# Kernel optimization log

Measured on AMD Instinct MI355X. Metric: run time of the kernel, lower is better.

Reference implementation:

```python
import jax, jax.numpy as jnp
import numpy as np

B, SQ, SK, D = 8, 4096, 4096, 64


def setup_inputs() -> dict:
    key = jax.random.key(0)
    k1, k2, k3 = jax.random.split(key, 3)
    x1 = jax.random.normal(k1, (B, SQ, D), dtype=jnp.float32)   # queries
    x2 = jax.random.normal(k2, (B, SK, D), dtype=jnp.float32)   # keys
    x3 = jax.random.normal(k3, (B, SK, D), dtype=jnp.float32)   # values
    x4 = 0                                                      # dropout p (static, 0 => deterministic)
    x5 = jnp.ones((1,), dtype=jnp.float32)                      # scale divisor
    return {"x1": x1, "x2": x2, "x3": x3, "x4": x4, "x5": x5}


def reference(x1, x2, x3, x4, x5):
    # scores: [B, Sq, Sk]
    scores = jnp.einsum("bqd,bkd->bqk", x1, x2) / x5
    attn = jax.nn.softmax(scores, axis=-1)
    p = float(x4)  # static python scalar
    if p > 0.0:
        mask = jax.random.bernoulli(jax.random.key(42), 1.0 - p, attn.shape)
        attn = attn * mask.astype(attn.dtype) / (1.0 - p)
    # out: [B, Sq, D]
    return jnp.einsum("bqk,bkd->bqd", attn, x3)
```

## Files before the change

kernel.cpp:

```cpp
#include <hip/hip_runtime.h>


typedef _Float16 f16x8 __attribute__((ext_vector_type(8)));
typedef _Float16 f16x4 __attribute__((ext_vector_type(4)));
typedef __fp16   h16x2 __attribute__((ext_vector_type(2)));
typedef float    f32x4 __attribute__((ext_vector_type(4)));
typedef float    f32x16 __attribute__((ext_vector_type(16)));

constexpr int kB  = 8;
constexpr int kSQ = 4096;
constexpr int kSK = 4096;
constexpr int kD  = 64;
constexpr int KSPLIT = 4;
constexpr int SKH = kSK / KSPLIT;
constexpr int BQ  = 128;
constexpr int BK  = 64;
constexpr size_t APART = (size_t)kB * kSQ * kD;
constexpr float kLog2e = 1.44269504088896340736f;

static __device__ __forceinline__ f16x4 pack4(float a, float b, float c, float d) {
    h16x2 p0 = __builtin_amdgcn_cvt_pkrtz(a, b);
    h16x2 p1 = __builtin_amdgcn_cvt_pkrtz(c, d);
    f16x4 r;
    r[0] = (_Float16)p0[0]; r[1] = (_Float16)p0[1];
    r[2] = (_Float16)p1[0]; r[3] = (_Float16)p1[1];
    return r;
}
static __device__ __forceinline__ f16x8 pack8(const float4& a, const float4& c) {
    f16x4 lo = pack4(a.x, a.y, a.z, a.w);
    f16x4 hi = pack4(c.x, c.y, c.z, c.w);
    f16x8 f;
    f[0] = lo[0]; f[1] = lo[1]; f[2] = lo[2]; f[3] = lo[3];
    f[4] = hi[0]; f[5] = hi[1]; f[6] = hi[2]; f[7] = hi[3];
    return f;
}
static __device__ __forceinline__ unsigned pkrtz_u(float a, float b) {
    union { h16x2 h; unsigned u; } cv;
    cv.h = __builtin_amdgcn_cvt_pkrtz(a, b);
    return cv.u;
}

typedef const __attribute__((address_space(1))) unsigned int* gu32p;
typedef __attribute__((address_space(3))) unsigned int* lu32p;
static __device__ __forceinline__ void gload_lds16(const void* g, void* l) {
    __builtin_amdgcn_global_load_lds((gu32p)g, (lu32p)l, 16, 0, 0);
}

#define PA_SLICE(dst, sv, rb) do {                                          \
    unsigned c0 = pkrtz_u((sv)[(rb)+0], (sv)[(rb)+1]);                      \
    unsigned c1 = pkrtz_u((sv)[(rb)+2], (sv)[(rb)+3]);                      \
    unsigned c2 = pkrtz_u((sv)[(rb)+4], (sv)[(rb)+5]);                      \
    unsigned c3 = pkrtz_u((sv)[(rb)+6], (sv)[(rb)+7]);                      \
    auto r02 = __builtin_amdgcn_permlane32_swap(c0, c2, false, false);      \
    auto r13 = __builtin_amdgcn_permlane32_swap(c1, c3, false, false);      \
    union { unsigned u[4]; f16x8 v; } _r;                                   \
    _r.u[0] = r02[0]; _r.u[1] = r13[0]; _r.u[2] = r02[1]; _r.u[3] = r13[1]; \
    dst = _r.v;                                                             \
} while (0)

__global__ __launch_bounds__(256, 2)
void fattn_prepass(const float* __restrict__ Kg,
                   const float* __restrict__ Vg,
                   _Float16* __restrict__ Kh,
                   _Float16* __restrict__ Vt)
{
    __shared__ _Float16 tr[kD][BK];

    const int tid = threadIdx.x;
    const int kt  = blockIdx.x;
    const int b   = blockIdx.y;

    const int k = tid >> 2;
    const int p = tid & 3;
    const int gk = kt * BK + k;

    {
        const float* src = Kg + ((size_t)b * kSK + gk) * kD + p * 16;
        const float4 a0 = *(const float4*)(src + 0);
        const float4 a1 = *(const float4*)(src + 4);
        const float4 a2 = *(const float4*)(src + 8);
        const float4 a3 = *(const float4*)(src + 12);
        _Float16* dst = Kh + ((size_t)b * kSK + gk) * kD;
        const int fb0 = 2 * p, fb1 = 2 * p + 1;
        *(f16x8*)&dst[(fb0 ^ (gk & 7)) * 8] = pack8(a0, a1);
        *(f16x8*)&dst[(fb1 ^ (gk & 7)) * 8] = pack8(a2, a3);
    }
    {
        const float* src = Vg + ((size_t)b * kSK + gk) * kD + p * 16;
        const float4 a0 = *(const float4*)(src + 0);
        const float4 a1 = *(const float4*)(src + 4);
        const float4 a2 = *(const float4*)(src + 8);
        const float4 a3 = *(const float4*)(src + 12);
        const float v[16] = {a0.x,a0.y,a0.z,a0.w, a1.x,a1.y,a1.z,a1.w,
                             a2.x,a2.y,a2.z,a2.w, a3.x,a3.y,a3.z,a3.w};
#pragma unroll
        for (int j = 0; j < 16; ++j)
            tr[p * 16 + j][k] = (_Float16)v[j];
    }
    __syncthreads();
    {
        const int f  = tid >> 2;
        const int p2 = tid & 3;
        const f16x8 b0 = *(const f16x8*)&tr[f][p2 * 16 + 0];
        const f16x8 b1 = *(const f16x8*)&tr[f][p2 * 16 + 8];
        _Float16* dst = Vt + (((size_t)b * 64 + kt) * kD + f) * BK;
        const int kb0 = 2 * p2, kb1 = 2 * p2 + 1;
        *(f16x8*)&dst[(kb0 ^ (f & 7)) * 8] = b0;
        *(f16x8*)&dst[(kb1 ^ (f & 7)) * 8] = b1;
    }
}

__global__ __launch_bounds__(256, 4)
void fattn_partial(const float* __restrict__ Qg,
                   const _Float16* __restrict__ Kh,
                   const _Float16* __restrict__ Vt,
                   const float* __restrict__ sdiv,
                   _Float16* __restrict__ Ap,
                   float2* __restrict__ MLp)
{
    __shared__ __align__(16) _Float16 sK[2][BK * kD];
    __shared__ __align__(16) _Float16 sV[2][kD * BK];

    const int tid  = threadIdx.x;
    const int w    = tid >> 6;
    const int lane = tid & 63;
    const int l31  = lane & 31;
    const int hi   = lane >> 5;

    const int flat = blockIdx.x;
    const int c    = flat & 31;
    const int qi   = flat >> 5;
    const int b    = c >> 2;
    const int ks   = c & 3;
    const int qb   = qi * BQ;

    const float qscale = kLog2e / sdiv[0];

    const float* Qb = Qg + ((size_t)b * kSQ + qb) * kD;
    const _Float16* Khb = Kh + ((size_t)b * kSK + (size_t)ks * SKH) * kD;
    const _Float16* Vtb = Vt + (((size_t)b * 64 + (size_t)ks * (SKH / BK)) * kD) * BK;

    f16x8 qf[4];
    {
        const float* qrow = Qb + (size_t)(w * 32 + l31) * kD;
#pragma unroll
        for (int ds = 0; ds < 4; ++ds) {
            const float4 a  = *(const float4*)(qrow + ds * 16 + hi * 8);
            const float4 cc = *(const float4*)(qrow + ds * 16 + hi * 8 + 4);
            float4 as = make_float4(a.x * qscale, a.y * qscale, a.z * qscale, a.w * qscale);
            float4 cs = make_float4(cc.x * qscale, cc.y * qscale, cc.z * qscale, cc.w * qscale);
            qf[ds] = pack8(as, cs);
        }
    }

    int offA[4];
#pragma unroll
    for (int i = 0; i < 4; ++i)
        offA[i] = l31 * 64 + (((2 * i + hi) ^ (l31 & 7)) * 8);

    auto stage = [&](int kt, int buf) {
        const char* gk = (const char*)(Khb + (size_t)kt * BK * kD) + w * 2048 + lane * 16;
        const char* gv = (const char*)(Vtb + (size_t)kt * kD * BK) + w * 2048 + lane * 16;
        char* lk = (char*)&sK[buf][0] + w * 2048;
        char* lv = (char*)&sV[buf][0] + w * 2048;
        gload_lds16(gk,        lk);
        gload_lds16(gk + 1024, lk + 1024);
        gload_lds16(gv,        lv);
        gload_lds16(gv + 1024, lv + 1024);
    };

    f32x16 o0, o1;
#pragma unroll
    for (int r = 0; r < 16; ++r) { o0[r] = 0.0f; o1[r] = 0.0f; }
    float m_i = -1e30f;
    float ll  = 0.0f;

    stage(0, 0);
    __syncthreads();

    const int nIter = SKH / BK;
    for (int kt = 0; kt < nIter; ++kt) {
        const int buf = kt & 1;
        if (kt + 1 < nIter) stage(kt + 1, buf ^ 1);

        f32x16 s0, s1;
#pragma unroll
        for (int r = 0; r < 16; ++r) { s0[r] = 0.0f; s1[r] = 0.0f; }
#pragma unroll
        for (int ds = 0; ds < 4; ++ds) {
            const f16x8 kf0 = *(const f16x8*)&sK[buf][offA[ds]];
            const f16x8 kf1 = *(const f16x8*)&sK[buf][offA[ds] + 2048];
            s0 = __builtin_amdgcn_mfma_f32_32x32x16_f16(kf0, qf[ds], s0, 0, 0, 0);
            s1 = __builtin_amdgcn_mfma_f32_32x32x16_f16(kf1, qf[ds], s1, 0, 0, 0);
        }

        f16x8 vf[4][2];
#pragma unroll
        for (int s = 0; s < 4; ++s) {
            vf[s][0] = *(const f16x8*)&sV[buf][offA[s]];
            vf[s][1] = *(const f16x8*)&sV[buf][offA[s] + 2048];
        }

        float t[16];
#pragma unroll
        for (int r = 0; r < 16; ++r) t[r] = fmaxf(s0[r], s1[r]);
#pragma unroll
        for (int r = 0; r < 8; ++r)  t[r] = fmaxf(t[r], t[r + 8]);
#pragma unroll
        for (int r = 0; r < 4; ++r)  t[r] = fmaxf(t[r], t[r + 4]);
        float rm = fmaxf(fmaxf(t[0], t[1]), fmaxf(t[2], t[3]));
        rm = fmaxf(rm, __shfl_xor(rm, 32, 64));
        const float mnew = fmaxf(m_i, rm);

#pragma unroll
        for (int r = 0; r < 16; ++r) {
            s0[r] = __builtin_amdgcn_exp2f(s0[r] - mnew);
            s1[r] = __builtin_amdgcn_exp2f(s1[r] - mnew);
        }
        if (!__all(mnew == m_i)) {
            const float alpha = __builtin_amdgcn_exp2f(m_i - mnew);
            ll *= alpha;
#pragma unroll
            for (int r = 0; r < 16; ++r) { o0[r] *= alpha; o1[r] *= alpha; }
        }
        m_i = mnew;

        {
            float a0 = 0.f, a1 = 0.f, a2 = 0.f, a3 = 0.f;
#pragma unroll
            for (int r = 0; r < 16; r += 4) {
                a0 += s0[r]; a1 += s0[r + 1]; a2 += s0[r + 2]; a3 += s0[r + 3];
                a0 += s1[r]; a1 += s1[r + 1]; a2 += s1[r + 2]; a3 += s1[r + 3];
            }
            ll += (a0 + a1) + (a2 + a3);
        }

        f16x8 pa[4];
        PA_SLICE(pa[0], s0, 0);
        PA_SLICE(pa[1], s0, 8);
        PA_SLICE(pa[2], s1, 0);
        PA_SLICE(pa[3], s1, 8);

#pragma unroll
        for (int s = 0; s < 4; ++s) {
            o0 = __builtin_amdgcn_mfma_f32_32x32x16_f16(vf[s][0], pa[s], o0, 0, 0, 0);
            o1 = __builtin_amdgcn_mfma_f32_32x32x16_f16(vf[s][1], pa[s], o1, 0, 0, 0);
        }

        __syncthreads();
    }

    _Float16* Ab = Ap + (size_t)ks * APART + ((size_t)b * kSQ + qb) * kD;
    float2* MLb = MLp + (size_t)ks * kB * kSQ + (size_t)b * kSQ + qb;
    const int q = w * 32 + l31;
    _Float16* arow = &Ab[(size_t)q * kD];
#pragma unroll
    for (int g = 0; g < 4; ++g) {
        *(f16x4*)&arow[g * 8 + hi * 4] =
            pack4(o0[4 * g], o0[4 * g + 1], o0[4 * g + 2], o0[4 * g + 3]);
        *(f16x4*)&arow[32 + g * 8 + hi * 4] =
            pack4(o1[4 * g], o1[4 * g + 1], o1[4 * g + 2], o1[4 * g + 3]);
    }
    {
        const float lf = ll + __shfl_xor(ll, 32, 64);
        if (hi == 0) MLb[q] = make_float2(m_i, lf);
    }
}

__global__ __launch_bounds__(256)
void fattn_combine(const _Float16* __restrict__ Ap,
                   const float2* __restrict__ MLp,
                   float* __restrict__ Og)
{
    const int idx = blockIdx.x * 256 + threadIdx.x;
    const int r = idx >> 4;
    const int c = (idx & 15) * 4;

    float m = -1e30f;
    float2 ml[KSPLIT];
#pragma unroll
    for (int s = 0; s < KSPLIT; ++s) {
        ml[s] = MLp[(size_t)s * kB * kSQ + r];
        m = fmaxf(m, ml[s].x);
    }
    float acc[4] = {0.f, 0.f, 0.f, 0.f};
    float lsum = 0.f;
#pragma unroll
    for (int s = 0; s < KSPLIT; ++s) {
        const float e = __builtin_amdgcn_exp2f(ml[s].x - m);
        lsum += e * ml[s].y;
        const f16x4 a = *(const f16x4*)&Ap[(size_t)s * APART + (size_t)r * kD + c];
#pragma unroll
        for (int j = 0; j < 4; ++j) acc[j] += e * (float)a[j];
    }
    const float inv = 1.0f / lsum;
    float4 res = make_float4(acc[0] * inv, acc[1] * inv, acc[2] * inv, acc[3] * inv);
    *(float4*)&Og[(size_t)r * kD + c] = res;
}

extern "C" void kernel_launch(void* const* d_in, const int* in_sizes, int n_in,
                              void* d_out, int out_size, void* d_ws, size_t ws_size,
                              hipStream_t stream) {
    const float* Q    = (const float*)d_in[0];
    const float* K    = (const float*)d_in[1];
    const float* V    = (const float*)d_in[2];
    const float* sdiv = (const float*)d_in[4];
    float* O = (float*)d_out;

    _Float16* Kh  = (_Float16*)d_ws;
    _Float16* Vt  = Kh + (size_t)kB * kSK * kD;
    _Float16* Ap  = Vt + (size_t)kB * kSK * kD;
    float2*   MLp = (float2*)(Ap + (size_t)KSPLIT * APART);

    fattn_prepass<<<dim3(kSK / BK, kB), dim3(256), 0, stream>>>(K, V, Kh, Vt);
    fattn_partial<<<dim3((kSQ / BQ) * kB * KSPLIT), dim3(256), 0, stream>>>(Q, Kh, Vt, sdiv, Ap, MLp);
    fattn_combine<<<dim3(kB * kSQ * kD / (256 * 4)), dim3(256), 0, stream>>>(Ap, MLp, O);
}
```

Before: 143.0 us.

## Double query tile per wave and defer softmax rescaling with a threshold

Each wave now processes two 32-row query tiles (BQ 256), reusing the V fragments loaded from LDS across both tiles and halving the number of workgroups. Online-softmax rescaling is skipped unless the new row max exceeds the running max by a threshold, which cuts rescale work and branch cost. Partial outputs are normalized before the fp16 store, and combine weights by exp*l so the fp16 partials stay in range. The cost is higher register pressure (occupancy hint lowered from 4 to 2), fewer blocks in flight, and K fragments are still reloaded per tile.

After: 135.0 us. 1.06x faster.

```diff
diff --git a/kernel.cpp b/kernel.cpp
--- a/kernel.cpp
+++ b/kernel.cpp
@@ -13,10 +13,12 @@
 constexpr int kD  = 64;
 constexpr int KSPLIT = 4;
 constexpr int SKH = kSK / KSPLIT;
-constexpr int BQ  = 128;
+constexpr int BQ  = 256;
+constexpr int MT  = 2;
 constexpr int BK  = 64;
 constexpr size_t APART = (size_t)kB * kSQ * kD;
 constexpr float kLog2e = 1.44269504088896340736f;
+constexpr float kDeferThr = 11.5f;
 
 static __device__ __forceinline__ f16x4 pack4(float a, float b, float c, float d) {
     h16x2 p0 = __builtin_amdgcn_cvt_pkrtz(a, b);
@@ -110,7 +112,7 @@
     }
 }
 
-__global__ __launch_bounds__(256, 4)
+__global__ __launch_bounds__(256, 2)
 void fattn_partial(const float* __restrict__ Qg,
                    const _Float16* __restrict__ Kh,
                    const _Float16* __restrict__ Vt,
@@ -140,16 +142,17 @@
     const _Float16* Khb = Kh + ((size_t)b * kSK + (size_t)ks * SKH) * kD;
     const _Float16* Vtb = Vt + (((size_t)b * 64 + (size_t)ks * (SKH / BK)) * kD) * BK;
 
-    f16x8 qf[4];
-    {
-        const float* qrow = Qb + (size_t)(w * 32 + l31) * kD;
+    f16x8 qf[MT][4];
+#pragma unroll
+    for (int mt = 0; mt < MT; ++mt) {
+        const float* qrow = Qb + (size_t)(w * 64 + mt * 32 + l31) * kD;
 #pragma unroll
         for (int ds = 0; ds < 4; ++ds) {
             const float4 a  = *(const float4*)(qrow + ds * 16 + hi * 8);
             const float4 cc = *(const float4*)(qrow + ds * 16 + hi * 8 + 4);
             float4 as = make_float4(a.x * qscale, a.y * qscale, a.z * qscale, a.w * qscale);
             float4 cs = make_float4(cc.x * qscale, cc.y * qscale, cc.z * qscale, cc.w * qscale);
-            qf[ds] = pack8(as, cs);
+            qf[mt][ds] = pack8(as, cs);
         }
     }
 
@@ -169,11 +172,14 @@
         gload_lds16(gv + 1024, lv + 1024);
     };
 
-    f32x16 o0, o1;
-#pragma unroll
-    for (int r = 0; r < 16; ++r) { o0[r] = 0.0f; o1[r] = 0.0f; }
-    float m_i = -1e30f;
-    float ll  = 0.0f;
+    f32x16 oL[MT], oH[MT];
+    float m_i[MT], ll[MT];
+#pragma unroll
+    for (int mt = 0; mt < MT; ++mt) {
+        m_i[mt] = -1e30f; ll[mt] = 0.0f;
+#pragma unroll
+        for (int r = 0; r < 16; ++r) { oL[mt][r] = 0.0f; oH[mt][r] = 0.0f; }
+    }
 
     stage(0, 0);
     __syncthreads();
@@ -183,17 +189,6 @@
         const int buf = kt & 1;
         if (kt + 1 < nIter) stage(kt + 1, buf ^ 1);
 
-        f32x16 s0, s1;
-#pragma unroll
-        for (int r = 0; r < 16; ++r) { s0[r] = 0.0f; s1[r] = 0.0f; }
-#pragma unroll
-        for (int ds = 0; ds < 4; ++ds) {
-            const f16x8 kf0 = *(const f16x8*)&sK[buf][offA[ds]];
-            const f16x8 kf1 = *(const f16x8*)&sK[buf][offA[ds] + 2048];
-            s0 = __builtin_amdgcn_mfma_f32_32x32x16_f16(kf0, qf[ds], s0, 0, 0, 0);
-            s1 = __builtin_amdgcn_mfma_f32_32x32x16_f16(kf1, qf[ds], s1, 0, 0, 0);
-        }
-
         f16x8 vf[4][2];
 #pragma unroll
         for (int s = 0; s < 4; ++s) {
@@ -201,50 +196,65 @@
             vf[s][1] = *(const f16x8*)&sV[buf][offA[s] + 2048];
         }
 
-        float t[16];
-#pragma unroll
-        for (int r = 0; r < 16; ++r) t[r] = fmaxf(s0[r], s1[r]);
-#pragma unroll
-        for (int r = 0; r < 8; ++r)  t[r] = fmaxf(t[r], t[r + 8]);
-#pragma unroll
-        for (int r = 0; r < 4; ++r)  t[r] = fmaxf(t[r], t[r + 4]);
-        float rm = fmaxf(fmaxf(t[0], t[1]), fmaxf(t[2], t[3]));
-        rm = fmaxf(rm, __shfl_xor(rm, 32, 64));
-        const float mnew = fmaxf(m_i, rm);
-
-#pragma unroll
-        for (int r = 0; r < 16; ++r) {
-            s0[r] = __builtin_amdgcn_exp2f(s0[r] - mnew);
-            s1[r] = __builtin_amdgcn_exp2f(s1[r] - mnew);
-        }
-        if (!__all(mnew == m_i)) {
-            const float alpha = __builtin_amdgcn_exp2f(m_i - mnew);
-            ll *= alpha;
-#pragma unroll
-            for (int r = 0; r < 16; ++r) { o0[r] *= alpha; o1[r] *= alpha; }
-        }
-        m_i = mnew;
-
-        {
-            float a0 = 0.f, a1 = 0.f, a2 = 0.f, a3 = 0.f;
-#pragma unroll
-            for (int r = 0; r < 16; r += 4) {
-                a0 += s0[r]; a1 += s0[r + 1]; a2 += s0[r + 2]; a3 += s0[r + 3];
-                a0 += s1[r]; a1 += s1[r + 1]; a2 += s1[r + 2]; a3 += s1[r + 3];
-            }
-            ll += (a0 + a1) + (a2 + a3);
-        }
-
-        f16x8 pa[4];
-        PA_SLICE(pa[0], s0, 0);
-        PA_SLICE(pa[1], s0, 8);
-        PA_SLICE(pa[2], s1, 0);
-        PA_SLICE(pa[3], s1, 8);
-
-#pragma unroll
-        for (int s = 0; s < 4; ++s) {
-            o0 = __builtin_amdgcn_mfma_f32_32x32x16_f16(vf[s][0], pa[s], o0, 0, 0, 0);
-            o1 = __builtin_amdgcn_mfma_f32_32x32x16_f16(vf[s][1], pa[s], o1, 0, 0, 0);
+#pragma unroll
+        for (int mt = 0; mt < MT; ++mt) {
+            f32x16 s0, s1;
+#pragma unroll
+            for (int r = 0; r < 16; ++r) { s0[r] = 0.0f; s1[r] = 0.0f; }
+#pragma unroll
+            for (int ds = 0; ds < 4; ++ds) {
+                const f16x8 kf0 = *(const f16x8*)&sK[buf][offA[ds]];
+                const f16x8 kf1 = *(const f16x8*)&sK[buf][offA[ds] + 2048];
+                s0 = __builtin_amdgcn_mfma_f32_32x32x16_f16(kf0, qf[mt][ds], s0, 0, 0, 0);
+                s1 = __builtin_amdgcn_mfma_f32_32x32x16_f16(kf1, qf[mt][ds], s1, 0, 0, 0);
+            }
+
+            float t[16];
+#pragma unroll
+            for (int r = 0; r < 16; ++r) t[r] = fmaxf(s0[r], s1[r]);
+#pragma unroll
+            for (int r = 0; r < 8; ++r)  t[r] = fmaxf(t[r], t[r + 8]);
+#pragma unroll
+            for (int r = 0; r < 4; ++r)  t[r] = fmaxf(t[r], t[r + 4]);
+            float rm = fmaxf(fmaxf(t[0], t[1]), fmaxf(t[2], t[3]));
+            rm = fmaxf(rm, __shfl_xor(rm, 32, 64));
+
+            if (!__all(rm <= m_i[mt] + kDeferThr)) {
+                const float mnew  = fmaxf(m_i[mt], rm);
+                const float alpha = __builtin_amdgcn_exp2f(m_i[mt] - mnew);
+                ll[mt] *= alpha;
+#pragma unroll
+                for (int r = 0; r < 16; ++r) { oL[mt][r] *= alpha; oH[mt][r] *= alpha; }
+                m_i[mt] = mnew;
+            }
+
+#pragma unroll
+            for (int r = 0; r < 16; ++r) {
+                s0[r] = __builtin_amdgcn_exp2f(s0[r] - m_i[mt]);
+                s1[r] = __builtin_amdgcn_exp2f(s1[r] - m_i[mt]);
+            }
+
+            {
+                float a0 = 0.f, a1 = 0.f, a2 = 0.f, a3 = 0.f;
+#pragma unroll
+                for (int r = 0; r < 16; r += 4) {
+                    a0 += s0[r]; a1 += s0[r + 1]; a2 += s0[r + 2]; a3 += s0[r + 3];
+                    a0 += s1[r]; a1 += s1[r + 1]; a2 += s1[r + 2]; a3 += s1[r + 3];
+                }
+                ll[mt] += (a0 + a1) + (a2 + a3);
+            }
+
+            f16x8 pa[4];
+            PA_SLICE(pa[0], s0, 0);
+            PA_SLICE(pa[1], s0, 8);
+            PA_SLICE(pa[2], s1, 0);
+            PA_SLICE(pa[3], s1, 8);
+
+#pragma unroll
+            for (int s = 0; s < 4; ++s) {
+                oL[mt] = __builtin_amdgcn_mfma_f32_32x32x16_f16(vf[s][0], pa[s], oL[mt], 0, 0, 0);
+                oH[mt] = __builtin_amdgcn_mfma_f32_32x32x16_f16(vf[s][1], pa[s], oH[mt], 0, 0, 0);
+            }
         }
 
         __syncthreads();
@@ -252,18 +262,22 @@
 
     _Float16* Ab = Ap + (size_t)ks * APART + ((size_t)b * kSQ + qb) * kD;
     float2* MLb = MLp + (size_t)ks * kB * kSQ + (size_t)b * kSQ + qb;
-    const int q = w * 32 + l31;
-    _Float16* arow = &Ab[(size_t)q * kD];
-#pragma unroll
-    for (int g = 0; g < 4; ++g) {
-        *(f16x4*)&arow[g * 8 + hi * 4] =
-            pack4(o0[4 * g], o0[4 * g + 1], o0[4 * g + 2], o0[4 * g + 3]);
-        *(f16x4*)&arow[32 + g * 8 + hi * 4] =
-            pack4(o1[4 * g], o1[4 * g + 1], o1[4 * g + 2], o1[4 * g + 3]);
-    }
-    {
-        const float lf = ll + __shfl_xor(ll, 32, 64);
-        if (hi == 0) MLb[q] = make_float2(m_i, lf);
+#pragma unroll
+    for (int mt = 0; mt < MT; ++mt) {
+        const int q = w * 64 + mt * 32 + l31;
+        const float lf = ll[mt] + __shfl_xor(ll[mt], 32, 64);
+        const float inv = 1.0f / lf;
+        _Float16* arow = &Ab[(size_t)q * kD];
+#pragma unroll
+        for (int g = 0; g < 4; ++g) {
+            *(f16x4*)&arow[g * 8 + hi * 4] =
+                pack4(oL[mt][4 * g] * inv, oL[mt][4 * g + 1] * inv,
+                      oL[mt][4 * g + 2] * inv, oL[mt][4 * g + 3] * inv);
+            *(f16x4*)&arow[32 + g * 8 + hi * 4] =
+                pack4(oH[mt][4 * g] * inv, oH[mt][4 * g + 1] * inv,
+                      oH[mt][4 * g + 2] * inv, oH[mt][4 * g + 3] * inv);
+        }
+        if (hi == 0) MLb[q] = make_float2(m_i[mt], lf);
     }
 }
 
@@ -287,11 +301,11 @@
     float lsum = 0.f;
 #pragma unroll
     for (int s = 0; s < KSPLIT; ++s) {
-        const float e = __builtin_amdgcn_exp2f(ml[s].x - m);
-        lsum += e * ml[s].y;
+        const float wgt = __builtin_amdgcn_exp2f(ml[s].x - m) * ml[s].y;
+        lsum += wgt;
         const f16x4 a = *(const f16x4*)&Ap[(size_t)s * APART + (size_t)r * kD + c];
 #pragma unroll
-        for (int j = 0; j < 4; ++j) acc[j] += e * (float)a[j];
+        for (int j = 0; j < 4; ++j) acc[j] += wgt * (float)a[j];
     }
     const float inv = 1.0f / lsum;
     float4 res = make_float4(acc[0] * inv, acc[1] * inv, acc[2] * inv, acc[3] * inv);
```
